# Performance work log

Measured on AMD Instinct MI355X. Metric: run time of the kernel, lower is better.

The kernel has to match this reference:

```python
import jax, jax.numpy as jnp
import numpy as np

N_NODE = 50000
N_EDGE = 800000
NODE_DIM, EDGE_DIM = 3, 4


def _relu(x):
    return jnp.maximum(x, 0)


def setup_inputs() -> dict:
    key = jax.random.key(0)
    ks = jax.random.split(key, 32)
    ki = iter(range(32))

    def w(shape):
        fan = shape[0]
        return (jax.random.normal(ks[next(ki)], shape, jnp.float32) / np.float32(np.sqrt(fan)))

    def b(n):
        return jnp.zeros((n,), jnp.float32)

    inp = {
        'nodes': jax.random.normal(ks[next(ki)], (N_NODE, NODE_DIM), jnp.float32),
        'edges': jax.random.normal(ks[next(ki)], (N_EDGE, EDGE_DIM), jnp.float32),
        'senders': jax.random.randint(ks[next(ki)], (N_EDGE,), 0, N_NODE, jnp.int32),
        'receivers': jax.random.randint(ks[next(ki)], (N_EDGE,), 0, N_NODE, jnp.int32),
        # psi1 encoder: [10 -> 256 -> 256 -> 128], relu after every layer (act_final=True)
        'mw0': w((NODE_DIM * 2 + EDGE_DIM, 256)), 'mb0': b(256),
        'mw1': w((256, 256)), 'mb1': b(256),
        'mw2': w((256, 128)), 'mb2': b(128),
        # psi2 attention: [128 -> 128 -> 128 -> 1], no final act
        'aw0': w((128, 128)), 'ab0': b(128),
        'aw1': w((128, 128)), 'ab1': b(128),
        'aw2': w((128, 1)), 'ab2': b(1),
        # psi3 value: [128 -> 256 -> 128], relu after every layer
        'vw0': w((128, 256)), 'vb0': b(256),
        'vw1': w((256, 128)), 'vb1': b(128),
        # psi4 decoder: [128 -> 256 -> 256 -> 1], no final act
        'uw0': w((128, 256)), 'ub0': b(256),
        'uw1': w((256, 256)), 'ub1': b(256),
        'uw2': w((256, 1)), 'ub2': b(1),
    }
    return inp


def reference(nodes, edges, senders, receivers,
              mw0, mb0, mw1, mb1, mw2, mb2,
              aw0, ab0, aw1, ab1, aw2, ab2,
              vw0, vb0, vw1, vb1,
              uw0, ub0, uw1, ub1, uw2, ub2):
    n_node = nodes.shape[0]
    # gather endpoint features and concat with edge features: (E, 2*node_dim+edge_dim)
    z = jnp.concatenate([nodes[senders], nodes[receivers], edges], axis=-1)
    # psi1 encoder (act_final=True)
    q = _relu(_relu(_relu(z @ mw0 + mb0) @ mw1 + mb1) @ mw2 + mb2)  # (E,128)
    # psi2 attention logits (no final act)
    w = (_relu(_relu(q @ aw0 + ab0) @ aw1 + ab1) @ aw2 + ab2)[:, 0]  # (E,)
    # segment softmax over receivers (matches torch scatter_reduce amax with -1e9 init)
    m = jax.ops.segment_max(w, receivers, num_segments=n_node)
    m = jnp.maximum(m, jnp.float32(-1e9))
    ex = jnp.exp(w - m[receivers])
    s = jax.ops.segment_sum(ex, receivers, num_segments=n_node)
    attn = ex / (s[receivers] + 1e-12)  # (E,)
    # psi3 value (act_final=True)
    v = _relu(_relu(q @ vw0 + vb0) @ vw1 + vb1)  # (E,128)
    # attention-weighted scatter-add aggregation to receiver nodes
    aggr = jax.ops.segment_sum(attn[:, None] * v, receivers, num_segments=n_node)  # (N,128)
    # psi4 decoder (no final act)
    out = _relu(_relu(aggr @ uw0 + ub0) @ uw1 + ub1) @ uw2 + ub2  # (N,1)
    return out
```

## Files before the change

kernel.cpp:

```cpp
#include <hip/hip_runtime.h>
#include <stdint.h>

#define NN_NODE 50000
#define NN_EDGE 800000

typedef _Float16 f16;
typedef _Float16 f16x2 __attribute__((ext_vector_type(2)));
typedef _Float16 f16x4 __attribute__((ext_vector_type(4)));
typedef _Float16 f16x8 __attribute__((ext_vector_type(8)));
typedef float f32x4 __attribute__((ext_vector_type(4)));

#define KEEP(x) asm volatile("" : "+v"(x))

#define WT_MW0   0
#define WT_MW1   8192
#define WT_MW2   73728
#define WT_AW0   106496
#define WT_AW1   122880
#define WT_VW0   139264
#define WT_VW1   172032
#define WT_UW0   204800
#define WT_UW1   237568
#define WT_TOTAL 303104

#define V_OFF      606208ull
#define WL_OFF     205406208ull
#define CNT_OFF    208606208ull
#define BASE_OFF   208806208ull
#define AGGR_OFF   209006208ull

__device__ __forceinline__ int swz(int row, int col) {
    return row * 256 + ((((col >> 3) ^ (row & 7))) << 3) + (col & 7);
}

__device__ __forceinline__ f16x2 pk2(float a, float b) {
    return __builtin_bit_cast(f16x2, __builtin_amdgcn_cvt_pkrtz(a, b));
}

template<int K, int N, int NKN, int EPI, int NW>
__device__ __forceinline__ void mlayer(const f16* in, int inoff,
        const f16* __restrict__ wt, const float* __restrict__ bias,
        f16* out, int outoff,
        f16x8* bf0, const f16* __restrict__ wtn, f16x8* bfn,
        const float* __restrict__ dvec, float* lpart,
        f16* __restrict__ vout, const int* sposp, int tid)
{
    const int wave = tid >> 6;
    const int lane = tid & 63;
    const int l15  = lane & 15;
    const int quad = lane >> 4;
    constexpr int NKS = K >> 5;
    constexpr int NCT = N >> 4;
    constexpr int ITC = NCT / NW;

    f16x8 af[4][NKS];
#pragma unroll
    for (int ms = 0; ms < 4; ++ms)
#pragma unroll
        for (int ks = 0; ks < NKS; ++ks) {
            af[ms][ks] = *(const f16x8*)(in + swz(ms * 16 + l15, inoff + ks * 32 + quad * 8));
            KEEP(af[ms][ks]);
        }

    if constexpr (NKN > 0) {
        const f16* wrow = wtn + (size_t)(wave * 16 + l15) * (NKN * 32) + quad * 8;
#pragma unroll
        for (int ks = 0; ks < NKN; ++ks) bfn[ks] = *(const f16x8*)(wrow + ks * 32);
    }

    int   sposv[4];
    float preg[4];
    if constexpr (EPI == 2) {
#pragma unroll
        for (int ms = 0; ms < 4; ++ms) sposv[ms] = sposp[ms * 16 + l15];
    }
    if constexpr (EPI == 1) {
#pragma unroll
        for (int ms = 0; ms < 4; ++ms) preg[ms] = 0.f;
    }

    f16x8 bfl[2][NKS > 0 ? NKS : 1];
#pragma unroll
    for (int ks = 0; ks < NKS; ++ks) bfl[0][ks] = bf0[ks];

#pragma unroll
    for (int i = 0; i < ITC; ++i) {
        const int ct = wave + i * NW;
        if (i + 1 < ITC) {
            const f16* wrow = wt + (size_t)((ct + NW) * 16 + l15) * K + quad * 8;
#pragma unroll
            for (int ks = 0; ks < NKS; ++ks)
                bfl[(i + 1) & 1][ks] = *(const f16x8*)(wrow + ks * 32);
        }
        const int f0 = ct * 16 + quad * 4;
        const float4 bv = *(const float4*)(bias + f0);
        float4 awv;
        if constexpr (EPI == 1) awv = *(const float4*)(dvec + f0);
#pragma unroll
        for (int ms = 0; ms < 4; ++ms) {
            f32x4 acc = {0.f, 0.f, 0.f, 0.f};
#pragma unroll
            for (int ks = 0; ks < NKS; ++ks)
                acc = __builtin_amdgcn_mfma_f32_16x16x32_f16(bfl[i & 1][ks], af[ms][ks], acc, 0, 0, 0);
            if constexpr (EPI == 1) {
                preg[ms] += fmaxf(acc[0] + bv.x, 0.f) * awv.x
                          + fmaxf(acc[1] + bv.y, 0.f) * awv.y
                          + fmaxf(acc[2] + bv.z, 0.f) * awv.z
                          + fmaxf(acc[3] + bv.w, 0.f) * awv.w;
            } else {
                f16x2 lo = pk2(fmaxf(acc[0] + bv.x, 0.f), fmaxf(acc[1] + bv.y, 0.f));
                f16x2 hi = pk2(fmaxf(acc[2] + bv.z, 0.f), fmaxf(acc[3] + bv.w, 0.f));
                f16x4 o; o[0] = lo[0]; o[1] = lo[1]; o[2] = hi[0]; o[3] = hi[1];
                if constexpr (EPI == 0)
                    *(f16x4*)(out + swz(ms * 16 + l15, outoff + f0)) = o;
                else
                    *(f16x4*)(vout + (size_t)sposv[ms] * 128 + f0) = o;
            }
        }
    }
    if constexpr (EPI == 1) {
#pragma unroll
        for (int ms = 0; ms < 4; ++ms) {
            float r = preg[ms];
            r += __shfl_xor(r, 16);
            r += __shfl_xor(r, 32);
            if (quad == 0) lpart[wave * 64 + ms * 16 + l15] = r;
        }
    }
}

struct WSeg { const float* src; int K, N, Kpad, dstOff; };
struct WSegs { WSeg s[9]; };

__global__ void prep_kernel(WSegs segs, f16* __restrict__ wt) {
    int idx = blockIdx.x * 256 + threadIdx.x;
    if (idx >= WT_TOTAL) return;
    int off = idx;
#pragma unroll
    for (int i = 0; i < 9; ++i) {
        int sz = segs.s[i].N * segs.s[i].Kpad;
        if (off < sz) {
            int n = off / segs.s[i].Kpad;
            int k = off - n * segs.s[i].Kpad;
            f16 val = (f16)0.f;
            if (k < segs.s[i].K) val = (f16)segs.s[i].src[k * segs.s[i].N + n];
            wt[segs.s[i].dstOff + off] = val;
            return;
        }
        off -= sz;
    }
}

__global__ void hist_kernel(const int* __restrict__ receivers, int* __restrict__ cnt) {
    int e = blockIdx.x * 256 + threadIdx.x;
    atomicAdd(&cnt[receivers[e]], 1);
}

__global__ __launch_bounds__(1024) void scan_kernel(int* __restrict__ cnt, int* __restrict__ base) {
    __shared__ int psum[1024];
    const int tid = threadIdx.x;
    const int CH = (NN_NODE + 1023) / 1024;
    const int lo = tid * CH;
    const int hi = min(lo + CH, NN_NODE);
    int s = 0;
    for (int i = lo; i < hi; ++i) s += cnt[i];
    psum[tid] = s;
    __syncthreads();
    for (int d = 1; d < 1024; d <<= 1) {
        int v = (tid >= d) ? psum[tid - d] : 0;
        __syncthreads();
        psum[tid] += v;
        __syncthreads();
    }
    int run = psum[tid] - s;
    for (int i = lo; i < hi; ++i) {
        int c = cnt[i];
        base[i] = run;
        cnt[i] = run;
        run += c;
    }
}

__global__ __launch_bounds__(256, 2) void edge_kernel(
        const float* __restrict__ nodes, const float* __restrict__ edges,
        const int* __restrict__ senders, const int* __restrict__ receivers,
        const f16* __restrict__ wt,
        const float* __restrict__ mb0, const float* __restrict__ mb1, const float* __restrict__ mb2,
        const float* __restrict__ ab0, const float* __restrict__ ab1,
        const float* __restrict__ aw2, const float* __restrict__ ab2,
        const float* __restrict__ vb0, const float* __restrict__ vb1,
        f16* __restrict__ vout, float* __restrict__ wlog, int* __restrict__ cursor)
{
    __shared__ f16 ldsbuf[2 * 64 * 256];
    __shared__ int spos[64];
    __shared__ float lpart[256];
    f16* bufA = ldsbuf;
    f16* bufB = ldsbuf + 64 * 256;
    const int tid = threadIdx.x;
    const int e0 = blockIdx.x * 64;
    const int wave = tid >> 6;
    const int lane = tid & 63;
    const int l15  = lane & 15;
    const int quad = lane >> 4;

    f16x8 bfA[8], bfB[8];

    {
        const f16* wrow = wt + WT_MW0 + (size_t)(wave * 16 + l15) * 32 + quad * 8;
        bfA[0] = *(const f16x8*)wrow;
    }

    {
        const int e = tid & 63, c = tid >> 6;
        f16x8 zv = {(f16)0.f,(f16)0.f,(f16)0.f,(f16)0.f,(f16)0.f,(f16)0.f,(f16)0.f,(f16)0.f};
        if (c == 0) {
            int s = senders[e0 + e];
            int r = receivers[e0 + e];
            const float2 ev = *(const float2*)(edges + (size_t)(e0 + e) * 4);
            zv[0] = (f16)nodes[s * 3 + 0]; zv[1] = (f16)nodes[s * 3 + 1]; zv[2] = (f16)nodes[s * 3 + 2];
            zv[3] = (f16)nodes[r * 3 + 0]; zv[4] = (f16)nodes[r * 3 + 1]; zv[5] = (f16)nodes[r * 3 + 2];
            zv[6] = (f16)ev.x; zv[7] = (f16)ev.y;
        } else if (c == 1) {
            const float2 ev = *(const float2*)(edges + (size_t)(e0 + e) * 4 + 2);
            zv[0] = (f16)ev.x; zv[1] = (f16)ev.y;
        }
        *(f16x8*)(bufA + e * 256 + ((c ^ (e & 7)) << 3)) = zv;
    }
    __syncthreads();

    mlayer< 32, 256, 8, 0, 4>(bufA, 0, wt + WT_MW0, mb0, bufB, 0, bfA, wt + WT_MW1, bfB,
                              nullptr, nullptr, nullptr, nullptr, tid);
    __syncthreads();
    mlayer<256, 256, 8, 0, 4>(bufB, 0, wt + WT_MW1, mb1, bufA, 0, bfB, wt + WT_MW2, bfA,
                              nullptr, nullptr, nullptr, nullptr, tid);
    __syncthreads();
    mlayer<256, 128, 4, 0, 4>(bufA, 0, wt + WT_MW2, mb2, bufB, 0, bfA, wt + WT_AW0, bfB,
                              nullptr, nullptr, nullptr, nullptr, tid);
    __syncthreads();
    mlayer<128, 128, 4, 0, 4>(bufB, 0, wt + WT_AW0, ab0, bufA, 0, bfB, wt + WT_AW1, bfA,
                              nullptr, nullptr, nullptr, nullptr, tid);
    __syncthreads();
    mlayer<128, 128, 4, 1, 4>(bufA, 0, wt + WT_AW1, ab1, nullptr, 0, bfA, wt + WT_VW0, bfB,
                              aw2, lpart, nullptr, nullptr, tid);
    __syncthreads();

    if (tid < 64) {
        float wv = ab2[0];
#pragma unroll
        for (int w = 0; w < 4; ++w) wv += lpart[w * 64 + tid];
        int r = receivers[e0 + tid];
        int pos = atomicAdd(&cursor[r], 1);
        spos[tid] = pos;
        wlog[pos] = wv;
    }
    mlayer<128, 256, 8, 0, 4>(bufB, 0, wt + WT_VW0, vb0, bufA, 0, bfB, wt + WT_VW1, bfA,
                              nullptr, nullptr, nullptr, nullptr, tid);
    __syncthreads();
    mlayer<256, 128, 0, 2, 4>(bufA, 0, wt + WT_VW1, vb1, nullptr, 0, bfA, nullptr, nullptr,
                              nullptr, nullptr, vout, spos, tid);
}

__global__ __launch_bounds__(256) void aggregate_kernel(
        const float* __restrict__ wlog, const f16* __restrict__ v,
        const int* __restrict__ base, float* __restrict__ aggr)
{
    const int tid = threadIdx.x;
    const int n = blockIdx.x * 4 + (tid >> 6);
    const int lane = tid & 63;
    int st = base[n];
    int en = (n == NN_NODE - 1) ? NN_EDGE : base[n + 1];
    st = max(0, min(st, NN_EDGE));
    en = max(st, min(en, NN_EDGE));

    float mx = -1e9f;
    for (int i = st + lane; i < en; i += 64) mx = fmaxf(mx, wlog[i]);
#pragma unroll
    for (int d = 1; d < 64; d <<= 1) mx = fmaxf(mx, __shfl_xor(mx, d));

    float sm = 0.f;
    for (int i = st + lane; i < en; i += 64) sm += __expf(wlog[i] - mx);
#pragma unroll
    for (int d = 1; d < 64; d <<= 1) sm += __shfl_xor(sm, d);
    const float inv = 1.f / (sm + 1e-12f);

    float acc0 = 0.f, acc1 = 0.f;
    const f16* vp = v + (size_t)st * 128 + lane * 2;
    for (int i = st; i < en; ++i, vp += 128) {
        float attn = __expf(wlog[i] - mx) * inv;
        f16x2 vv = *(const f16x2*)vp;
        acc0 += attn * (float)vv[0];
        acc1 += attn * (float)vv[1];
    }
    float2 o; o.x = acc0; o.y = acc1;
    *(float2*)(aggr + (size_t)n * 128 + lane * 2) = o;
}

__global__ __launch_bounds__(256, 2) void node_kernel(
        const float* __restrict__ aggr, const f16* __restrict__ wt,
        const float* __restrict__ ub0, const float* __restrict__ ub1,
        const float* __restrict__ uw2, const float* __restrict__ ub2,
        float* __restrict__ out)
{
    __shared__ f16 ldsbuf[2 * 64 * 256];
    __shared__ float lpart[256];
    f16* bufA = ldsbuf;
    f16* bufB = ldsbuf + 64 * 256;
    const int tid = threadIdx.x;
    const int n0 = blockIdx.x * 64;
    const int wave = tid >> 6;
    const int lane = tid & 63;
    const int l15  = lane & 15;
    const int quad = lane >> 4;

    f16x8 bfA[8], bfB[8];
    {
        const f16* wrow = wt + WT_UW0 + (size_t)(wave * 16 + l15) * 128 + quad * 8;
#pragma unroll
        for (int ks = 0; ks < 4; ++ks) bfA[ks] = *(const f16x8*)(wrow + ks * 32);
    }

    {
        int row = tid >> 2, j = tid & 3;
        int n = n0 + row;
#pragma unroll
        for (int c2 = 0; c2 < 4; ++c2) {
            f16x8 p;
            if (n < NN_NODE) {
                const float4* src = (const float4*)(aggr + (size_t)n * 128 + j * 32 + c2 * 8);
                float4 a = src[0], b = src[1];
                f16x2 q0 = pk2(a.x, a.y), q1 = pk2(a.z, a.w);
                f16x2 q2 = pk2(b.x, b.y), q3 = pk2(b.z, b.w);
                p[0]=q0[0]; p[1]=q0[1]; p[2]=q1[0]; p[3]=q1[1];
                p[4]=q2[0]; p[5]=q2[1]; p[6]=q3[0]; p[7]=q3[1];
            } else {
                p = (f16x8)(f16)0.f;
            }
            int chunk = j * 4 + c2;
            *(f16x8*)(bufA + row * 256 + ((chunk ^ (row & 7)) << 3)) = p;
        }
    }
    __syncthreads();

    mlayer<128, 256, 8, 0, 4>(bufA, 0, wt + WT_UW0, ub0, bufB, 0, bfA, wt + WT_UW1, bfB,
                              nullptr, nullptr, nullptr, nullptr, tid);
    __syncthreads();
    mlayer<256, 256, 0, 1, 4>(bufB, 0, wt + WT_UW1, ub1, nullptr, 0, bfB, nullptr, nullptr,
                              uw2, lpart, nullptr, nullptr, tid);
    __syncthreads();
    if (tid < 64) {
        float sum = ub2[0];
#pragma unroll
        for (int w = 0; w < 4; ++w) sum += lpart[w * 64 + tid];
        int n = n0 + tid;
        if (n < NN_NODE) out[n] = sum;
    }
}

extern "C" void kernel_launch(void* const* d_in, const int* in_sizes, int n_in,
                              void* d_out, int out_size, void* d_ws, size_t ws_size,
                              hipStream_t stream)
{
    const float* nodes     = (const float*)d_in[0];
    const float* edges     = (const float*)d_in[1];
    const int*   senders   = (const int*)d_in[2];
    const int*   receivers = (const int*)d_in[3];
    const float* mw0 = (const float*)d_in[4];  const float* mb0 = (const float*)d_in[5];
    const float* mw1 = (const float*)d_in[6];  const float* mb1 = (const float*)d_in[7];
    const float* mw2 = (const float*)d_in[8];  const float* mb2 = (const float*)d_in[9];
    const float* aw0 = (const float*)d_in[10]; const float* ab0 = (const float*)d_in[11];
    const float* aw1 = (const float*)d_in[12]; const float* ab1 = (const float*)d_in[13];
    const float* aw2 = (const float*)d_in[14]; const float* ab2 = (const float*)d_in[15];
    const float* vw0 = (const float*)d_in[16]; const float* vb0 = (const float*)d_in[17];
    const float* vw1 = (const float*)d_in[18]; const float* vb1 = (const float*)d_in[19];
    const float* uw0 = (const float*)d_in[20]; const float* ub0 = (const float*)d_in[21];
    const float* uw1 = (const float*)d_in[22]; const float* ub1 = (const float*)d_in[23];
    const float* uw2 = (const float*)d_in[24]; const float* ub2 = (const float*)d_in[25];

    char* ws = (char*)d_ws;
    f16*   wt   = (f16*)ws;
    f16*   vbuf = (f16*)(ws + V_OFF);
    float* wlog = (float*)(ws + WL_OFF);
    int*   cnt  = (int*)(ws + CNT_OFF);
    int*   base = (int*)(ws + BASE_OFF);
    float* aggr = (float*)(ws + AGGR_OFF);
    float* out  = (float*)d_out;

    (void)hipMemsetAsync(cnt, 0, NN_NODE * sizeof(int), stream);

    WSegs segs = {{
        { mw0,  10, 256,  32, WT_MW0 },
        { mw1, 256, 256, 256, WT_MW1 },
        { mw2, 256, 128, 256, WT_MW2 },
        { aw0, 128, 128, 128, WT_AW0 },
        { aw1, 128, 128, 128, WT_AW1 },
        { vw0, 128, 256, 128, WT_VW0 },
        { vw1, 256, 128, 256, WT_VW1 },
        { uw0, 128, 256, 128, WT_UW0 },
        { uw1, 256, 256, 256, WT_UW1 },
    }};
    prep_kernel<<<(WT_TOTAL + 255) / 256, 256, 0, stream>>>(segs, wt);

    hist_kernel<<<NN_EDGE / 256, 256, 0, stream>>>(receivers, cnt);
    scan_kernel<<<1, 1024, 0, stream>>>(cnt, base);

    edge_kernel<<<NN_EDGE / 64, 256, 0, stream>>>(nodes, edges, senders, receivers, wt,
        mb0, mb1, mb2, ab0, ab1, aw2, ab2, vb0, vb1, vbuf, wlog, cnt);

    aggregate_kernel<<<NN_NODE / 4, 256, 0, stream>>>(wlog, vbuf, base, aggr);

    node_kernel<<<(NN_NODE + 63) / 64, 256, 0, stream>>>(aggr, wt, ub0, ub1, uw2, ub2, out);
}
```

Measured before the change: 1.005 ms.

## Split MLP layers across eight waves by edge half and column group

Edge and node kernels now launch 512 threads (8 waves) per block. Each wave handles 32 of the 64 rows and a quarter of the output column tiles, so it holds half as many A fragments. Weight B fragments are no longer double-buffered in registers, and the KEEP asm barriers are removed. The aim is to lower per-wave register pressure and raise the number of waves hiding latency, at the cost of each weight fragment being loaded by two waves and less prefetch overlap.

```diff
diff --git a/kernel.cpp b/kernel.cpp
--- a/kernel.cpp
+++ b/kernel.cpp
@@ -9,8 +9,6 @@
 typedef _Float16 f16x4 __attribute__((ext_vector_type(4)));
 typedef _Float16 f16x8 __attribute__((ext_vector_type(8)));
 typedef float f32x4 __attribute__((ext_vector_type(4)));
-
-#define KEEP(x) asm volatile("" : "+v"(x))
 
 #define WT_MW0   0
 #define WT_MW1   8192
@@ -37,8 +35,8 @@
     return __builtin_bit_cast(f16x2, __builtin_amdgcn_cvt_pkrtz(a, b));
 }
 
-template<int K, int N, int NKN, int EPI, int NW>
-__device__ __forceinline__ void mlayer(const f16* in, int inoff,
+template<int K, int N, int NKN, int EPI>
+__device__ __forceinline__ void mlayer8(const f16* in, int inoff,
         const f16* __restrict__ wt, const float* __restrict__ bias,
         f16* out, int outoff,
         f16x8* bf0, const f16* __restrict__ wtn, f16x8* bfn,
@@ -46,62 +44,63 @@
         f16* __restrict__ vout, const int* sposp, int tid)
 {
     const int wave = tid >> 6;
+    const int eh   = wave >> 2;
+    const int ctg  = wave & 3;
     const int lane = tid & 63;
     const int l15  = lane & 15;
     const int quad = lane >> 4;
     constexpr int NKS = K >> 5;
     constexpr int NCT = N >> 4;
-    constexpr int ITC = NCT / NW;
-
-    f16x8 af[4][NKS];
-#pragma unroll
-    for (int ms = 0; ms < 4; ++ms)
-#pragma unroll
-        for (int ks = 0; ks < NKS; ++ks) {
-            af[ms][ks] = *(const f16x8*)(in + swz(ms * 16 + l15, inoff + ks * 32 + quad * 8));
-            KEEP(af[ms][ks]);
-        }
+    constexpr int ITC = NCT / 4;
+
+    f16x8 af[2][NKS];
+#pragma unroll
+    for (int ms = 0; ms < 2; ++ms)
+#pragma unroll
+        for (int ks = 0; ks < NKS; ++ks)
+            af[ms][ks] = *(const f16x8*)(in + swz(eh * 32 + ms * 16 + l15,
+                                                  inoff + ks * 32 + quad * 8));
 
     if constexpr (NKN > 0) {
-        const f16* wrow = wtn + (size_t)(wave * 16 + l15) * (NKN * 32) + quad * 8;
+        const f16* wrow = wtn + (size_t)(ctg * 16 + l15) * (NKN * 32) + quad * 8;
 #pragma unroll
         for (int ks = 0; ks < NKN; ++ks) bfn[ks] = *(const f16x8*)(wrow + ks * 32);
     }
 
-    int   sposv[4];
-    float preg[4];
+    int   sposv[2];
+    float preg[2];
     if constexpr (EPI == 2) {
 #pragma unroll
-        for (int ms = 0; ms < 4; ++ms) sposv[ms] = sposp[ms * 16 + l15];
+        for (int ms = 0; ms < 2; ++ms) sposv[ms] = sposp[eh * 32 + ms * 16 + l15];
     }
     if constexpr (EPI == 1) {
 #pragma unroll
-        for (int ms = 0; ms < 4; ++ms) preg[ms] = 0.f;
-    }
-
-    f16x8 bfl[2][NKS > 0 ? NKS : 1];
-#pragma unroll
-    for (int ks = 0; ks < NKS; ++ks) bfl[0][ks] = bf0[ks];
+        for (int ms = 0; ms < 2; ++ms) preg[ms] = 0.f;
+    }
+
+    f16x8 bfl[NKS];
+#pragma unroll
+    for (int ks = 0; ks < NKS; ++ks) bfl[ks] = bf0[ks];
 
 #pragma unroll
     for (int i = 0; i < ITC; ++i) {
-        const int ct = wave + i * NW;
-        if (i + 1 < ITC) {
-            const f16* wrow = wt + (size_t)((ct + NW) * 16 + l15) * K + quad * 8;
+        const int ct = ctg + i * 4;
+        if (i > 0) {
+            const f16* wrow = wt + (size_t)(ct * 16 + l15) * K + quad * 8;
 #pragma unroll
             for (int ks = 0; ks < NKS; ++ks)
-                bfl[(i + 1) & 1][ks] = *(const f16x8*)(wrow + ks * 32);
+                bfl[ks] = *(const f16x8*)(wrow + ks * 32);
         }
         const int f0 = ct * 16 + quad * 4;
         const float4 bv = *(const float4*)(bias + f0);
         float4 awv;
         if constexpr (EPI == 1) awv = *(const float4*)(dvec + f0);
 #pragma unroll
-        for (int ms = 0; ms < 4; ++ms) {
+        for (int ms = 0; ms < 2; ++ms) {
             f32x4 acc = {0.f, 0.f, 0.f, 0.f};
 #pragma unroll
             for (int ks = 0; ks < NKS; ++ks)
-                acc = __builtin_amdgcn_mfma_f32_16x16x32_f16(bfl[i & 1][ks], af[ms][ks], acc, 0, 0, 0);
+                acc = __builtin_amdgcn_mfma_f32_16x16x32_f16(bfl[ks], af[ms][ks], acc, 0, 0, 0);
             if constexpr (EPI == 1) {
                 preg[ms] += fmaxf(acc[0] + bv.x, 0.f) * awv.x
                           + fmaxf(acc[1] + bv.y, 0.f) * awv.y
@@ -112,7 +111,7 @@
                 f16x2 hi = pk2(fmaxf(acc[2] + bv.z, 0.f), fmaxf(acc[3] + bv.w, 0.f));
                 f16x4 o; o[0] = lo[0]; o[1] = lo[1]; o[2] = hi[0]; o[3] = hi[1];
                 if constexpr (EPI == 0)
-                    *(f16x4*)(out + swz(ms * 16 + l15, outoff + f0)) = o;
+                    *(f16x4*)(out + swz(eh * 32 + ms * 16 + l15, outoff + f0)) = o;
                 else
                     *(f16x4*)(vout + (size_t)sposv[ms] * 128 + f0) = o;
             }
@@ -120,11 +119,11 @@
     }
     if constexpr (EPI == 1) {
 #pragma unroll
-        for (int ms = 0; ms < 4; ++ms) {
+        for (int ms = 0; ms < 2; ++ms) {
             float r = preg[ms];
             r += __shfl_xor(r, 16);
             r += __shfl_xor(r, 32);
-            if (quad == 0) lpart[wave * 64 + ms * 16 + l15] = r;
+            if (quad == 0) lpart[wave * 32 + ms * 16 + l15] = r;
         }
     }
 }
@@ -181,7 +180,7 @@
     }
 }
 
-__global__ __launch_bounds__(256, 2) void edge_kernel(
+__global__ __launch_bounds__(512, 4) void edge_kernel(
         const float* __restrict__ nodes, const float* __restrict__ edges,
         const int* __restrict__ senders, const int* __restrict__ receivers,
         const f16* __restrict__ wt,
@@ -199,6 +198,7 @@
     const int tid = threadIdx.x;
     const int e0 = blockIdx.x * 64;
     const int wave = tid >> 6;
+    const int ctg  = wave & 3;
     const int lane = tid & 63;
     const int l15  = lane & 15;
     const int quad = lane >> 4;
@@ -206,11 +206,11 @@
     f16x8 bfA[8], bfB[8];
 
     {
-        const f16* wrow = wt + WT_MW0 + (size_t)(wave * 16 + l15) * 32 + quad * 8;
+        const f16* wrow = wt + WT_MW0 + (size_t)(ctg * 16 + l15) * 32 + quad * 8;
         bfA[0] = *(const f16x8*)wrow;
     }
 
-    {
+    if (tid < 256) {
         const int e = tid & 63, c = tid >> 6;
         f16x8 zv = {(f16)0.f,(f16)0.f,(f16)0.f,(f16)0.f,(f16)0.f,(f16)0.f,(f16)0.f,(f16)0.f};
         if (c == 0) {
@@ -228,36 +228,37 @@
     }
     __syncthreads();
 
-    mlayer< 32, 256, 8, 0, 4>(bufA, 0, wt + WT_MW0, mb0, bufB, 0, bfA, wt + WT_MW1, bfB,
-                              nullptr, nullptr, nullptr, nullptr, tid);
-    __syncthreads();
-    mlayer<256, 256, 8, 0, 4>(bufB, 0, wt + WT_MW1, mb1, bufA, 0, bfB, wt + WT_MW2, bfA,
-                              nullptr, nullptr, nullptr, nullptr, tid);
-    __syncthreads();
-    mlayer<256, 128, 4, 0, 4>(bufA, 0, wt + WT_MW2, mb2, bufB, 0, bfA, wt + WT_AW0, bfB,
-                              nullptr, nullptr, nullptr, nullptr, tid);
-    __syncthreads();
-    mlayer<128, 128, 4, 0, 4>(bufB, 0, wt + WT_AW0, ab0, bufA, 0, bfB, wt + WT_AW1, bfA,
-                              nullptr, nullptr, nullptr, nullptr, tid);
-    __syncthreads();
-    mlayer<128, 128, 4, 1, 4>(bufA, 0, wt + WT_AW1, ab1, nullptr, 0, bfA, wt + WT_VW0, bfB,
-                              aw2, lpart, nullptr, nullptr, tid);
+    mlayer8< 32, 256, 8, 0>(bufA, 0, wt + WT_MW0, mb0, bufB, 0, bfA, wt + WT_MW1, bfB,
+                            nullptr, nullptr, nullptr, nullptr, tid);
+    __syncthreads();
+    mlayer8<256, 256, 8, 0>(bufB, 0, wt + WT_MW1, mb1, bufA, 0, bfB, wt + WT_MW2, bfA,
+                            nullptr, nullptr, nullptr, nullptr, tid);
+    __syncthreads();
+    mlayer8<256, 128, 4, 0>(bufA, 0, wt + WT_MW2, mb2, bufB, 0, bfA, wt + WT_AW0, bfB,
+                            nullptr, nullptr, nullptr, nullptr, tid);
+    __syncthreads();
+    mlayer8<128, 128, 4, 0>(bufB, 0, wt + WT_AW0, ab0, bufA, 0, bfB, wt + WT_AW1, bfA,
+                            nullptr, nullptr, nullptr, nullptr, tid);
+    __syncthreads();
+    mlayer8<128, 128, 4, 1>(bufA, 0, wt + WT_AW1, ab1, nullptr, 0, bfA, wt + WT_VW0, bfB,
+                            aw2, lpart, nullptr, nullptr, tid);
     __syncthreads();
 
     if (tid < 64) {
+        const int eh = tid >> 5, r32 = tid & 31;
         float wv = ab2[0];
 #pragma unroll
-        for (int w = 0; w < 4; ++w) wv += lpart[w * 64 + tid];
+        for (int g = 0; g < 4; ++g) wv += lpart[(eh * 4 + g) * 32 + r32];
         int r = receivers[e0 + tid];
         int pos = atomicAdd(&cursor[r], 1);
         spos[tid] = pos;
         wlog[pos] = wv;
     }
-    mlayer<128, 256, 8, 0, 4>(bufB, 0, wt + WT_VW0, vb0, bufA, 0, bfB, wt + WT_VW1, bfA,
-                              nullptr, nullptr, nullptr, nullptr, tid);
-    __syncthreads();
-    mlayer<256, 128, 0, 2, 4>(bufA, 0, wt + WT_VW1, vb1, nullptr, 0, bfA, nullptr, nullptr,
-                              nullptr, nullptr, vout, spos, tid);
+    mlayer8<128, 256, 8, 0>(bufB, 0, wt + WT_VW0, vb0, bufA, 0, bfB, wt + WT_VW1, bfA,
+                            nullptr, nullptr, nullptr, nullptr, tid);
+    __syncthreads();
+    mlayer8<256, 128, 0, 2>(bufA, 0, wt + WT_VW1, vb1, nullptr, 0, bfA, nullptr, nullptr,
+                            nullptr, nullptr, vout, spos, tid);
 }
 
 __global__ __launch_bounds__(256) void aggregate_kernel(
@@ -295,7 +296,7 @@
     *(float2*)(aggr + (size_t)n * 128 + lane * 2) = o;
 }
 
-__global__ __launch_bounds__(256, 2) void node_kernel(
+__global__ __launch_bounds__(512, 4) void node_kernel(
         const float* __restrict__ aggr, const f16* __restrict__ wt,
         const float* __restrict__ ub0, const float* __restrict__ ub1,
         const float* __restrict__ uw2, const float* __restrict__ ub2,
@@ -308,18 +309,19 @@
     const int tid = threadIdx.x;
     const int n0 = blockIdx.x * 64;
     const int wave = tid >> 6;
+    const int ctg  = wave & 3;
     const int lane = tid & 63;
     const int l15  = lane & 15;
     const int quad = lane >> 4;
 
     f16x8 bfA[8], bfB[8];
     {
-        const f16* wrow = wt + WT_UW0 + (size_t)(wave * 16 + l15) * 128 + quad * 8;
+        const f16* wrow = wt + WT_UW0 + (size_t)(ctg * 16 + l15) * 128 + quad * 8;
 #pragma unroll
         for (int ks = 0; ks < 4; ++ks) bfA[ks] = *(const f16x8*)(wrow + ks * 32);
     }
 
-    {
+    if (tid < 256) {
         int row = tid >> 2, j = tid & 3;
         int n = n0 + row;
 #pragma unroll
@@ -341,16 +343,17 @@
     }
     __syncthreads();
 
-    mlayer<128, 256, 8, 0, 4>(bufA, 0, wt + WT_UW0, ub0, bufB, 0, bfA, wt + WT_UW1, bfB,
-                              nullptr, nullptr, nullptr, nullptr, tid);
-    __syncthreads();
-    mlayer<256, 256, 0, 1, 4>(bufB, 0, wt + WT_UW1, ub1, nullptr, 0, bfB, nullptr, nullptr,
-                              uw2, lpart, nullptr, nullptr, tid);
+    mlayer8<128, 256, 8, 0>(bufA, 0, wt + WT_UW0, ub0, bufB, 0, bfA, wt + WT_UW1, bfB,
+                            nullptr, nullptr, nullptr, nullptr, tid);
+    __syncthreads();
+    mlayer8<256, 256, 0, 1>(bufB, 0, wt + WT_UW1, ub1, nullptr, 0, bfB, nullptr, nullptr,
+                            uw2, lpart, nullptr, nullptr, tid);
     __syncthreads();
     if (tid < 64) {
+        const int eh = tid >> 5, r32 = tid & 31;
         float sum = ub2[0];
 #pragma unroll
-        for (int w = 0; w < 4; ++w) sum += lpart[w * 64 + tid];
+        for (int g = 0; g < 4; ++g) sum += lpart[(eh * 4 + g) * 32 + r32];
         int n = n0 + tid;
         if (n < NN_NODE) out[n] = sum;
     }
@@ -403,10 +406,10 @@
     hist_kernel<<<NN_EDGE / 256, 256, 0, stream>>>(receivers, cnt);
     scan_kernel<<<1, 1024, 0, stream>>>(cnt, base);
 
-    edge_kernel<<<NN_EDGE / 64, 256, 0, stream>>>(nodes, edges, senders, receivers, wt,
+    edge_kernel<<<NN_EDGE / 64, 512, 0, stream>>>(nodes, edges, senders, receivers, wt,
         mb0, mb1, mb2, ab0, ab1, aw2, ab2, vb0, vb1, vbuf, wlog, cnt);
 
     aggregate_kernel<<<NN_NODE / 4, 256, 0, stream>>>(wlog, vbuf, base, aggr);
 
-    node_kernel<<<(NN_NODE + 63) / 64, 256, 0, stream>>>(aggr, wt, ub0, ub1, uw2, ub2, out);
-}
+    node_kernel<<<(NN_NODE + 63) / 64, 512, 0, stream>>>(aggr, wt, ub0, ub1, uw2, ub2, out);
+}
```

After: 1.533 ms. 1.53x slower.
